# Performance work log

Hardware: AMD Instinct MI355X
Metric: run time of the kernel (lower is better)

Reference implementation:

```python
import jax, jax.numpy as jnp
import numpy as np
from jax import lax

B, C, H, W = 16, 256, 32, 32
HK, WK = 16, 16
NH = 8              # num_heads
HD = C // NH        # head_dim = 32
N = H * W           # 1024
M = HK * WK         # 256
EXP = 3             # attn_expansion
HID = NH * EXP      # 24 hidden channels in DLA
EPS = 1e-5


def setup_inputs() -> dict:
    key = jax.random.key(0)
    ks = jax.random.split(key, 16)
    s = 0.02
    return {
        "q": jax.random.normal(ks[0], (B, C, H, W), jnp.float32),
        "kv": jax.random.normal(ks[1], (B, C, HK, WK), jnp.float32),
        "Wq": jax.random.normal(ks[2], (C, C), jnp.float32) * s,
        "Wkv": jax.random.normal(ks[3], (2 * C, C), jnp.float32) * s,
        "Wp": jax.random.normal(ks[4], (C, C), jnp.float32) * s,
        "bp": jnp.zeros((C,), jnp.float32),
        "rpb": jnp.ones((N, M), jnp.float32),
        "W_exp": jax.random.normal(ks[5], (HID, NH), jnp.float32) * s,   # 1x1 conv heads->hidden
        "g1": jnp.ones((HID,), jnp.float32),
        "b1": jnp.zeros((HID,), jnp.float32),
        "W_dw": jax.random.normal(ks[6], (HID, 1, 3, 3), jnp.float32) * s,  # depthwise 3x3
        "g2": jnp.ones((HID,), jnp.float32),
        "b2": jnp.zeros((HID,), jnp.float32),
        "W_red": jax.random.normal(ks[7], (NH, HID), jnp.float32) * s,  # 1x1 conv hidden->heads
        "g3": jnp.ones((NH,), jnp.float32),
        "b3": jnp.zeros((NH,), jnp.float32),
    }


def group_norm(x, gamma, beta, groups):
    b, c, h, w = x.shape
    xg = x.reshape(b, groups, c // groups, h, w)
    mu = xg.mean(axis=(2, 3, 4), keepdims=True)
    var = xg.var(axis=(2, 3, 4), keepdims=True)
    xn = ((xg - mu) * lax.rsqrt(var + EPS)).reshape(b, c, h, w)
    return xn * gamma[None, :, None, None] + beta[None, :, None, None]


def swish(x):
    return x * jax.nn.sigmoid(x)


def dla(a, W_exp, g1, b1, W_dw, g2, b2, W_red, g3, b3):
    # a: [B, NH, N, M] treated as NCHW image with C=num_heads
    x = jnp.einsum('bcnm,oc->bonm', a, W_exp)              # 1x1 expand -> [B,HID,N,M]
    x = swish(group_norm(x, g1, b1, EXP))
    x = lax.conv_general_dilated(
        x, W_dw, window_strides=(1, 1), padding='SAME',
        feature_group_count=HID,
        dimension_numbers=('NCHW', 'OIHW', 'NCHW'))        # depthwise 3x3
    x = swish(group_norm(x, g2, b2, EXP))
    x = jnp.einsum('bcnm,oc->bonm', x, W_red)              # 1x1 reduce -> [B,NH,N,M]
    x = group_norm(x, g3, b3, 1)                            # no activation
    return x


def reference(q, kv, Wq, Wkv, Wp, bp, rpb, W_exp, g1, b1, W_dw, g2, b2, W_red, g3, b3):
    b = q.shape[0]
    scale = HD ** -0.5
    # kv path: [B,C,HK,WK] -> [B,M,C] -> Linear(C->2C)
    kv_t = kv.reshape(b, C, M).transpose(0, 2, 1)
    kvp = kv_t @ Wkv.T                                     # [B,M,2C]
    kvp = kvp.reshape(b, M, 2, NH, HD).transpose(2, 0, 3, 1, 4)  # [2,B,NH,M,HD]
    k, v = kvp[0], kvp[1]
    # q path: [B,C,H,W] -> [B,N,C] -> Linear -> [B,NH,N,HD]
    qf = (q.reshape(b, C, N).transpose(0, 2, 1) @ Wq.T)
    qh = qf.reshape(b, N, NH, HD).transpose(0, 2, 1, 3)
    attn = jnp.einsum('bhnd,bhmd->bhnm', qh, k) * scale + rpb[None, None]
    attn = jax.nn.softmax(attn, axis=-1)
    attn = dla(attn, W_exp, g1, b1, W_dw, g2, b2, W_red, g3, b3)
    out = jnp.einsum('bhnm,bhmd->bhnd', attn, v)           # [B,NH,N,HD]
    out = out.transpose(0, 2, 1, 3).reshape(b, N, C)
    out = out @ Wp.T + bp
    return out.transpose(0, 2, 1).reshape(b, C, H, W)
```

## Files before the change

### kernel.cpp

```cpp
#include <hip/hip_runtime.h>
#include <math.h>

#define Bb 16
#define Cc 256
#define Nn 1024
#define Mm 256
#define NHh 8
#define HDd 32
#define HIDh 24
#define NMs (Nn*Mm)
#define TTB 16
#define CHUNK 8
#define EPSf 1e-5f
#define SCALEf 0.17677669529663687f
#define STP 32

typedef float v2f __attribute__((ext_vector_type(2)));
typedef __attribute__((ext_vector_type(8))) short bf8v;
typedef __attribute__((ext_vector_type(4))) float f4v;

__device__ __forceinline__ float wave_sum(float v){
#pragma unroll
  for (int off=32; off; off>>=1) v += __shfl_xor(v, off, 64);
  return v;
}
__device__ __forceinline__ float wave_max(float v){
#pragma unroll
  for (int off=32; off; off>>=1) v = fmaxf(v, __shfl_xor(v, off, 64));
  return v;
}
__device__ __forceinline__ float sigm_(float x){ return __builtin_amdgcn_rcpf(1.f + __expf(-x)); }
__device__ __forceinline__ float swish_(float x){ return x * sigm_(x); }
__device__ __forceinline__ v2f swish2(v2f x){
  v2f r;
  r.x = x.x * sigm_(x.x);
  r.y = x.y * sigm_(x.y);
  return r;
}
__device__ __forceinline__ unsigned short f2bf(float f){
  unsigned u = __float_as_uint(f);
  u += 0x7fffu + ((u >> 16) & 1u);
  return (unsigned short)(u >> 16);
}
__device__ __forceinline__ unsigned cvtpk(float lo, float hi){
  unsigned r;
  asm("v_cvt_pk_bf16_f32 %0, %1, %2" : "=v"(r) : "v"(lo), "v"(hi));
  return r;
}
__device__ __forceinline__ float bfup(unsigned short s){ return __uint_as_float(((unsigned)s) << 16); }
__device__ __forceinline__ float bflo(unsigned u){ return __uint_as_float(u << 16); }
__device__ __forceinline__ float bfhi(unsigned u){ return __uint_as_float(u & 0xffff0000u); }
__device__ __forceinline__ void gload_lds16(const void* g, void* l){
  __builtin_amdgcn_global_load_lds(
      (const __attribute__((address_space(1))) unsigned int*)g,
      (__attribute__((address_space(3))) unsigned int*)l, 16, 0, 0);
}

template<int HASBIAS>
__launch_bounds__(256)
__global__ void gemm_mfma(const float* __restrict__ A,
                          const float* __restrict__ W,
                          const float* __restrict__ bias,
                          float* __restrict__ O)
{
  __shared__ __align__(16) unsigned short Wt[64 * 40];
  __shared__ __align__(16) unsigned short At[64 * 40];
  const int b = blockIdx.z;
  const int i0 = blockIdx.x * 64;
  const int j0 = blockIdx.y * 64;
  const int tid = threadIdx.x;
  const int lane = tid & 63, wv = tid >> 6;
  const int wj = (wv >> 1) * 32, wi = (wv & 1) * 32;
  const int l15 = lane & 15, l4 = lane >> 4;

  const float* Ab = A + (long)b * Cc * Nn;
  const int sj = tid >> 2, skh = (tid & 3) * 8;
  const int si = tid & 63, skb = (tid >> 6) * 8;

  f4v acc[2][2] = {};
  for (int k0 = 0; k0 < Cc; k0 += 32) {
    float wreg[8];
    {
      const float* wp = W + (long)(j0 + sj) * Cc + k0 + skh;
      *(f4v*)&wreg[0] = *(const f4v*)&wp[0];
      *(f4v*)&wreg[4] = *(const f4v*)&wp[4];
    }
    float areg[8];
    {
      const float* ap = Ab + (long)(k0 + skb) * Nn + i0 + si;
#pragma unroll
      for (int e = 0; e < 8; e++) areg[e] = ap[(long)e * Nn];
    }
    __syncthreads();
    {
      unsigned pk[4];
#pragma unroll
      for (int t = 0; t < 4; t++) pk[t] = cvtpk(wreg[2*t], wreg[2*t+1]);
      *(uint4*)&Wt[sj*40 + skh] = make_uint4(pk[0], pk[1], pk[2], pk[3]);
#pragma unroll
      for (int t = 0; t < 4; t++) pk[t] = cvtpk(areg[2*t], areg[2*t+1]);
      *(uint4*)&At[si*40 + skb] = make_uint4(pk[0], pk[1], pk[2], pk[3]);
    }
    __syncthreads();
    bf8v af[2], bf[2];
#pragma unroll
    for (int fm = 0; fm < 2; fm++)
      af[fm] = *(const bf8v*)&Wt[(wj + fm*16 + l15)*40 + l4*8];
#pragma unroll
    for (int fn = 0; fn < 2; fn++)
      bf[fn] = *(const bf8v*)&At[(wi + fn*16 + l15)*40 + l4*8];
#pragma unroll
    for (int fm = 0; fm < 2; fm++)
#pragma unroll
      for (int fn = 0; fn < 2; fn++)
        acc[fm][fn] = __builtin_amdgcn_mfma_f32_16x16x32_bf16(af[fm], bf[fn], acc[fm][fn], 0, 0, 0);
  }
#pragma unroll
  for (int fm = 0; fm < 2; fm++) {
    f4v bv = {0.f, 0.f, 0.f, 0.f};
    if (HASBIAS) bv = *(const f4v*)&bias[j0 + wj + fm*16 + l4*4];
#pragma unroll
    for (int fn = 0; fn < 2; fn++) {
      const int jj = j0 + wj + fm*16 + l4*4;
      const int ii = i0 + wi + fn*16 + l15;
      float* op = O + ((long)b * Cc + jj) * Nn + ii;
#pragma unroll
      for (int r = 0; r < 4; r++)
        op[(long)r * Nn] = acc[fm][fn][r] + bv[r];
    }
  }
}

template<int MODE>
__launch_bounds__(256)
__global__ void gemm_tn(const float* __restrict__ A, const float* __restrict__ W,
                        const float* __restrict__ bias, float* __restrict__ O1,
                        float* __restrict__ O2, int Kdim, long sAb, int sAk, int sAi)
{
  __shared__ __align__(16) float As[16][68];
  __shared__ __align__(16) float Ws[16][68];
  const int b  = blockIdx.z;
  const int i0 = blockIdx.x * 64;
  const int j0 = blockIdx.y * 64;
  const int tid = threadIdx.x;
  const int tx = tid & 15, ty = tid >> 4;
  const float* Ab = A + (long)b * sAb;
  float acc[4][4] = {};
  for (int k0 = 0; k0 < Kdim; k0 += 16) {
#pragma unroll
    for (int t = 0; t < 4; t++) {
      int idx = tid + t * 256;
      int kk, ii;
      if (sAi == 1) { kk = idx >> 6; ii = idx & 63; }
      else          { ii = idx >> 4; kk = idx & 15; }
      As[kk][ii] = Ab[(long)(k0 + kk) * sAk + (long)(i0 + ii) * sAi];
    }
#pragma unroll
    for (int t = 0; t < 4; t++) {
      int idx = tid + t * 256;
      int jj = idx & 63, kk = idx >> 6;
      Ws[kk][jj] = W[(long)(j0 + jj) * Kdim + (k0 + kk)];
    }
    __syncthreads();
#pragma unroll
    for (int kk = 0; kk < 16; kk++) {
      const float4 av = *(const float4*)&As[kk][tx * 4];
      const float4 wv = *(const float4*)&Ws[kk][ty * 4];
      const float a4[4] = {av.x, av.y, av.z, av.w};
      const float w4[4] = {wv.x, wv.y, wv.z, wv.w};
#pragma unroll
      for (int u = 0; u < 4; u++)
#pragma unroll
        for (int v = 0; v < 4; v++)
          acc[u][v] = fmaf(a4[u], w4[v], acc[u][v]);
    }
    __syncthreads();
  }
#pragma unroll
  for (int v = 0; v < 4; v++) {
    const int j = j0 + ty * 4 + v;
    const int two = j >> 8, jj = j & 255;
    const int h = jj >> 5, d = jj & 31;
    float* p = two ? O2 : O1;
#pragma unroll
    for (int u = 0; u < 4; u++)
      p[(((long)b * NHh + h) * Mm + (i0 + tx * 4 + u)) * HDd + d] = acc[u][v];
  }
}

__launch_bounds__(256)
__global__ void compute_sv(const float* __restrict__ vb, float* __restrict__ sv)
{
  __shared__ float red[256];
  const int bh = blockIdx.x, tid = threadIdx.x;
  const int d = tid & 31, ch = tid >> 5;
  const float* vp = vb + (long)bh * Mm * HDd;
  float s = 0.f;
  for (int m = ch; m < Mm; m += 8) s += vp[m * HDd + d];
  red[tid] = s;
  __syncthreads();
  if (tid < 32) {
    float t = 0.f;
#pragma unroll
    for (int cc = 0; cc < 8; cc++) t += red[cc * 32 + tid];
    sv[(long)bh * HDd + tid] = t;
  }
}

__launch_bounds__(256)
__global__ void attn_softmax(const float* __restrict__ qhT, const float* __restrict__ kb,
                             const float* __restrict__ rpb, unsigned short* __restrict__ attn)
{
  __shared__ __align__(16) float Ks[Mm][36];
  __shared__ __align__(16) float qs[32][36];
  const int b = blockIdx.z, h = blockIdx.y, n0 = blockIdx.x * 32;
  const int tid = threadIdx.x;
  const float* kp = kb + ((long)b * NHh + h) * Mm * HDd;
#pragma unroll
  for (int u = 0; u < 8; u++) {
    const int f = tid + u * 256;
    const int m = f >> 3, d = (f & 7) * 4;
    *(float4*)&Ks[m][d] = *(const float4*)&kp[m * HDd + d];
  }
  const float* qp = qhT + ((long)b * NHh + h) * HDd * Nn;
#pragma unroll
  for (int u = 0; u < 4; u++) {
    const int idx = tid + u * 256;
    const int nn = idx & 31, dd = idx >> 5;
    qs[nn][dd] = qp[(long)dd * Nn + n0 + nn];
  }
  __syncthreads();
  const int lane = tid & 63, w = tid >> 6;
  const int r0 = w * 8;
  float s[8][4] = {};
#pragma unroll
  for (int dq = 0; dq < 8; dq++) {
    float4 k4[4];
#pragma unroll
    for (int j = 0; j < 4; j++) k4[j] = *(const float4*)&Ks[lane + j * 64][dq * 4];
#pragma unroll
    for (int r = 0; r < 8; r++) {
      const float4 q4 = *(const float4*)&qs[r0 + r][dq * 4];
#pragma unroll
      for (int j = 0; j < 4; j++) {
        s[r][j] = fmaf(q4.x, k4[j].x, s[r][j]);
        s[r][j] = fmaf(q4.y, k4[j].y, s[r][j]);
        s[r][j] = fmaf(q4.z, k4[j].z, s[r][j]);
        s[r][j] = fmaf(q4.w, k4[j].w, s[r][j]);
      }
    }
  }
#pragma unroll
  for (int r = 0; r < 8; r++) {
    const int n = n0 + r0 + r;
    const float* rp = rpb + (long)n * Mm;
    float sc[4];
#pragma unroll
    for (int j = 0; j < 4; j++) sc[j] = fmaf(s[r][j], SCALEf, rp[lane + j * 64]);
    float mx = fmaxf(fmaxf(sc[0], sc[1]), fmaxf(sc[2], sc[3]));
    mx = wave_max(mx);
    float e[4], sum = 0.f;
#pragma unroll
    for (int j = 0; j < 4; j++) { e[j] = __expf(sc[j] - mx); sum += e[j]; }
    sum = wave_sum(sum);
    const float inv = __builtin_amdgcn_rcpf(sum);
    unsigned short* ap = attn + (((long)b * NHh + h) * Nn + n) * Mm;
#pragma unroll
    for (int j = 0; j < 4; j++) ap[lane + j * 64] = f2bf(e[j] * inv);
  }
}

__launch_bounds__(256)
__global__ void gram_stats(const unsigned short* __restrict__ attn, float* __restrict__ G)
{
  __shared__ float red[36][4];
  const int b = blockIdx.y, tid = threadIdx.x;
  const unsigned short* ap = attn + (long)b * NHh * NMs + (long)blockIdx.x * 2048 + tid * 8;
  float a[8][8];
#pragma unroll
  for (int h = 0; h < 8; h++) {
    const uint4 v = *(const uint4*)&ap[(long)h * NMs];
    a[h][0] = bflo(v.x); a[h][1] = bfhi(v.x); a[h][2] = bflo(v.y); a[h][3] = bfhi(v.y);
    a[h][4] = bflo(v.z); a[h][5] = bfhi(v.z); a[h][6] = bflo(v.w); a[h][7] = bfhi(v.w);
  }
  float g[36];
  int t = 0;
#pragma unroll
  for (int i = 0; i < 8; i++)
#pragma unroll
    for (int j = i; j < 8; j++, t++) {
      float s = 0.f;
#pragma unroll
      for (int m = 0; m < 8; m++) s = fmaf(a[i][m], a[j][m], s);
      g[t] = s;
    }
  const int lane = tid & 63, wid = tid >> 6;
#pragma unroll
  for (int t2 = 0; t2 < 36; t2++) {
    const float s = wave_sum(g[t2]);
    if (lane == 0) red[t2][wid] = s;
  }
  __syncthreads();
  if (tid < 36)
    atomicAdd(&G[((long)b * 36 + tid) * STP],
              red[tid][0] + red[tid][1] + red[tid][2] + red[tid][3]);
}

__launch_bounds__(768, 6)
__global__ void dla_pass_b(const unsigned short* __restrict__ attn,
                           const float* __restrict__ Wexp,
                           const float* __restrict__ g1, const float* __restrict__ b1,
                           const float* __restrict__ G, const float* __restrict__ Wdw,
                           unsigned short* __restrict__ x2, float* __restrict__ stats2c, int b0)
{
  __shared__ __align__(16) unsigned short sl[(TTB + 2) * NHh * Mm];
  const int tid = threadIdx.x;
  const int wv = tid >> 6, lane = tid & 63;
  const int bc = blockIdx.y, b = b0 + bc;
  const int n0 = blockIdx.x * TTB;
  const int c0 = wv * 2;
  const int g = wv >> 2;

  {
    const unsigned short* abase = attn + (long)b * NHh * NMs;
    const int q_lo = lane >> 5;
    const int m0 = (lane & 31) * 8;
#pragma unroll
    for (int i = 0; i < 6; i++) {
      const int pp = (wv * 6 + i) * 2;
      const int row = pp >> 3;
      const int nn = n0 - 1 + row;
      if (nn >= 0 && nn < Nn) {
        const int h = (pp + q_lo) & 7;
        gload_lds16(abase + (long)h * NMs + (long)nn * Mm + m0, &sl[pp * Mm]);
      }
    }
  }

  float mu, rs;
  {
    const float* Gb = G + (long)b * 36 * STP;
    float sum = 0.f, sumsq = 0.f;
    for (int c = g * 8; c < g * 8 + 8; c++) {
      float w[8];
#pragma unroll
      for (int h = 0; h < 8; h++) w[h] = Wexp[c * 8 + h];
      float wsu = 0.f;
#pragma unroll
      for (int h = 0; h < 8; h++) wsu += w[h];
      sum += wsu;
      float s2 = 0.f;
      int t = 0;
#pragma unroll
      for (int i = 0; i < 8; i++)
#pragma unroll
        for (int j = i; j < 8; j++, t++) {
          const float f = (i == j) ? 1.f : 2.f;
          s2 = fmaf(f * w[i] * w[j], Gb[t * STP], s2);
        }
      sumsq += s2;
    }
    const float cnt = 8.f * NMs;
    mu = sum * ((float)Nn / cnt);
    const float var = sumsq / cnt - mu * mu;
    rs = rsqrtf(var + EPSf);
  }
  v2f we2[8], wd2[9], B12;
  {
    const float A10 = rs * g1[c0], A11 = rs * g1[c0 + 1];
    B12.x = b1[c0] - mu * A10;
    B12.y = b1[c0 + 1] - mu * A11;
#pragma unroll
    for (int h = 0; h < NHh; h++) {
      we2[h].x = Wexp[c0 * NHh + h] * A10;
      we2[h].y = Wexp[(c0 + 1) * NHh + h] * A11;
    }
#pragma unroll
    for (int k = 0; k < 9; k++) {
      wd2[k].x = Wdw[c0 * 9 + k];
      wd2[k].y = Wdw[(c0 + 1) * 9 + k];
    }
  }
  __syncthreads();

  v2f s1p[4] = {}, s2p[4] = {};
  v2f smp = {0.f, 0.f}, sqp = {0.f, 0.f};
  for (int r = -1; r <= TTB; r++) {
    const int nn = n0 + r;
    const bool rowv = (nn >= 0 && nn < Nn);
    v2f xp[4];
    if (rowv) {
#pragma unroll
      for (int mi = 0; mi < 4; mi++) xp[mi] = B12;
      const unsigned short* sp = &sl[(r + 1) * NHh * Mm + lane * 4];
#pragma unroll
      for (int h = 0; h < NHh; h++) {
        const ushort4 v = *(const ushort4*)&sp[h * Mm];
        xp[0] += we2[h] * bfup(v.x);
        xp[1] += we2[h] * bfup(v.y);
        xp[2] += we2[h] * bfup(v.z);
        xp[3] += we2[h] * bfup(v.w);
      }
#pragma unroll
      for (int mi = 0; mi < 4; mi++) xp[mi] = swish2(xp[mi]);
    } else {
#pragma unroll
      for (int mi = 0; mi < 4; mi++) xp[mi] = (v2f){0.f, 0.f};
    }
    v2f xl, xr;
    xl.x = __shfl_up(xp[3].x, 1);  xl.y = __shfl_up(xp[3].y, 1);
    xr.x = __shfl_down(xp[0].x, 1); xr.y = __shfl_down(xp[0].y, 1);
    if (lane == 0)  { xl = (v2f){0.f, 0.f}; }
    if (lane == 63) { xr = (v2f){0.f, 0.f}; }
    const v2f L[4] = {xl, xp[0], xp[1], xp[2]};
    const v2f R[4] = {xp[1], xp[2], xp[3], xr};
    v2f y[4];
#pragma unroll
    for (int mi = 0; mi < 4; mi++) {
      const v2f u0 = wd2[0] * L[mi] + wd2[1] * xp[mi] + wd2[2] * R[mi];
      const v2f u1 = wd2[3] * L[mi] + wd2[4] * xp[mi] + wd2[5] * R[mi];
      const v2f u2 = wd2[6] * L[mi] + wd2[7] * xp[mi] + wd2[8] * R[mi];
      y[mi] = s2p[mi] + u2;
      s2p[mi] = s1p[mi] + u1;
      s1p[mi] = u0;
    }
    if (r >= 1) {
#pragma unroll
      for (int mi = 0; mi < 4; mi++) {
        smp += y[mi];
        sqp += y[mi] * y[mi];
      }
      const int nw = n0 + r - 1;
      const unsigned w0 = cvtpk(y[0].x, y[1].x), w1 = cvtpk(y[2].x, y[3].x);
      const unsigned w2 = cvtpk(y[0].y, y[1].y), w3 = cvtpk(y[2].y, y[3].y);
      unsigned short* xq = x2 + ((long)(bc * Nn + nw) * HIDh + c0) * Mm + lane * 4;
      *(uint2*)xq        = make_uint2(w0, w1);
      *(uint2*)(xq + Mm) = make_uint2(w2, w3);
    }
  }
  {
    const float vs0 = wave_sum(smp.x), vq0 = wave_sum(sqp.x);
    const float vs1 = wave_sum(smp.y), vq1 = wave_sum(sqp.y);
    if (lane == 0) {
      atomicAdd(&stats2c[((long)b * HIDh + c0) * STP], vs0);
      atomicAdd(&stats2c[((long)b * HIDh + c0) * STP + 1], vq0);
      atomicAdd(&stats2c[((long)b * HIDh + c0 + 1) * STP], vs1);
      atomicAdd(&stats2c[((long)b * HIDh + c0 + 1) * STP + 1], vq1);
    }
  }
}

__launch_bounds__(256)
__global__ void dla_pass_c(const unsigned short* __restrict__ x2, const float* __restrict__ g2,
                           const float* __restrict__ b2, const float* __restrict__ stats2c,
                           const float* __restrict__ Wred, unsigned short* __restrict__ a2,
                           float* __restrict__ partial3, int b0)
{
  __shared__ float wA[HIDh], wB[HIDh], wrs[HIDh][NHh];
  __shared__ float red2[2][4];
  const int tid = threadIdx.x;
  const int wv = tid >> 6, lane = tid & 63;
  const int bc = blockIdx.y, b = b0 + bc;
  if (tid < HIDh) {
    const int c = tid, g = c >> 3;
    float s = 0.f, q = 0.f;
#pragma unroll
    for (int cc = 0; cc < 8; cc++) {
      s += stats2c[((long)b * HIDh + g * 8 + cc) * STP];
      q += stats2c[((long)b * HIDh + g * 8 + cc) * STP + 1];
    }
    const float cnt = 8.f * NMs;
    const float mu = s / cnt;
    const float var = q / cnt - mu * mu;
    const float A2 = rsqrtf(var + EPSf) * g2[c];
    wA[c] = A2; wB[c] = b2[c] - mu * A2;
  }
  if (tid < HIDh * NHh) {
    const int c = tid >> 3, h = tid & 7;
    wrs[c][h] = Wred[h * HIDh + c];
  }
  __syncthreads();
  const int rsel = lane >> 5, ms = lane & 31;
  const int n = blockIdx.x * 8 + wv * 2 + rsel;
  const unsigned short* xp = x2 + (long)(bc * Nn + n) * HIDh * Mm + ms * 8;
  float red[NHh][8] = {};
#pragma unroll
  for (int c = 0; c < HIDh; c++) {
    const uint4 xv = *(const uint4*)&xp[c * Mm];
    const float Ac = wA[c], Bc = wB[c];
    float sw[8];
    sw[0] = swish_(fmaf(bflo(xv.x), Ac, Bc));
    sw[1] = swish_(fmaf(bfhi(xv.x), Ac, Bc));
    sw[2] = swish_(fmaf(bflo(xv.y), Ac, Bc));
    sw[3] = swish_(fmaf(bfhi(xv.y), Ac, Bc));
    sw[4] = swish_(fmaf(bflo(xv.z), Ac, Bc));
    sw[5] = swish_(fmaf(bfhi(xv.z), Ac, Bc));
    sw[6] = swish_(fmaf(bflo(xv.w), Ac, Bc));
    sw[7] = swish_(fmaf(bfhi(xv.w), Ac, Bc));
#pragma unroll
    for (int h = 0; h < NHh; h++) {
      const float w = wrs[c][h];
#pragma unroll
      for (int mi = 0; mi < 8; mi++) red[h][mi] = fmaf(w, sw[mi], red[h][mi]);
    }
  }
  float s3 = 0.f, q3 = 0.f;
#pragma unroll
  for (int h = 0; h < NHh; h++) {
    uint4 st;
    st.x = cvtpk(red[h][0], red[h][1]);
    st.y = cvtpk(red[h][2], red[h][3]);
    st.z = cvtpk(red[h][4], red[h][5]);
    st.w = cvtpk(red[h][6], red[h][7]);
    *(uint4*)&a2[(((long)b * NHh + h) * Nn + n) * Mm + ms * 8] = st;
#pragma unroll
    for (int mi = 0; mi < 8; mi++) {
      s3 += red[h][mi]; q3 = fmaf(red[h][mi], red[h][mi], q3);
    }
  }
  s3 = wave_sum(s3); q3 = wave_sum(q3);
  if (lane == 0) { red2[0][wv] = s3; red2[1][wv] = q3; }
  __syncthreads();
  if (tid < 2) {
    float t = red2[tid][0] + red2[tid][1] + red2[tid][2] + red2[tid][3];
    partial3[((long)b * 128 + blockIdx.x) * 2 + tid] = t;
  }
}

__launch_bounds__(128)
__global__ void finalize_stats3(const float* __restrict__ partial3, float* __restrict__ stats3)
{
  __shared__ float red2[2][2];
  const int b = blockIdx.x, tid = threadIdx.x;
  const int lane = tid & 63, wv = tid >> 6;
  float s = partial3[((long)b * 128 + tid) * 2];
  float q = partial3[((long)b * 128 + tid) * 2 + 1];
  s = wave_sum(s); q = wave_sum(q);
  if (lane == 0) { red2[0][wv] = s; red2[1][wv] = q; }
  __syncthreads();
  if (tid < 2)
    stats3[b * 2 + tid] = red2[tid][0] + red2[tid][1];
}

__launch_bounds__(256)
__global__ void pv_mfma(const unsigned short* __restrict__ a2, const float* __restrict__ vb,
                        const float* __restrict__ sv, const float* __restrict__ stats3,
                        const float* __restrict__ g3, const float* __restrict__ b3,
                        float* __restrict__ o)
{
  __shared__ __align__(16) unsigned short Vt[32 * 264];
  const int b = blockIdx.z, h = blockIdx.y, n0 = blockIdx.x * 128;
  const int tid = threadIdx.x;
  const int lane = tid & 63, wv = tid >> 6;
  const int l15 = lane & 15, l4 = lane >> 4;
  {
    const float* vp = vb + ((long)b * NHh + h) * Mm * HDd;
#pragma unroll
    for (int u = 0; u < 32; u++) {
      const int idx = tid + u * 256;
      const int m = idx >> 5, d = idx & 31;
      Vt[d * 264 + m] = f2bf(vp[idx]);
    }
  }
  __syncthreads();
  const unsigned short* ap = a2 + (((long)b * NHh + h) * Nn + n0) * Mm;
  f4v acc[2][2] = {};
#pragma unroll 2
  for (int k0 = 0; k0 < Mm; k0 += 32) {
    bf8v af[2], bf[2];
#pragma unroll
    for (int fm = 0; fm < 2; fm++)
      af[fm] = *(const bf8v*)&Vt[(fm * 16 + l15) * 264 + k0 + l4 * 8];
#pragma unroll
    for (int fn = 0; fn < 2; fn++)
      bf[fn] = *(const bf8v*)&ap[(long)(wv * 32 + fn * 16 + l15) * Mm + k0 + l4 * 8];
#pragma unroll
    for (int fm = 0; fm < 2; fm++)
#pragma unroll
      for (int fn = 0; fn < 2; fn++)
        acc[fm][fn] = __builtin_amdgcn_mfma_f32_16x16x32_bf16(af[fm], bf[fn], acc[fm][fn], 0, 0, 0);
  }
  const float cnt = (float)(NHh * NMs);
  const float mu = stats3[b * 2] / cnt;
  const float var = stats3[b * 2 + 1] / cnt - mu * mu;
  const float r3 = rsqrtf(var + EPSf);
  const float alpha = r3 * g3[h];
  const float beta = b3[h] - mu * alpha;
#pragma unroll
  for (int fm = 0; fm < 2; fm++) {
#pragma unroll
    for (int r = 0; r < 4; r++) {
      const int d = fm * 16 + l4 * 4 + r;
      const float bv = beta * sv[((long)b * NHh + h) * HDd + d];
      float* op = o + ((long)b * Cc + h * HDd + d) * Nn + n0 + wv * 32 + l15;
#pragma unroll
      for (int fn = 0; fn < 2; fn++)
        op[fn * 16] = fmaf(alpha, acc[fm][fn][r], bv);
    }
  }
}

extern "C" void kernel_launch(void* const* d_in, const int* in_sizes, int n_in,
                              void* d_out, int out_size, void* d_ws, size_t ws_size,
                              hipStream_t stream) {
  const float* q    = (const float*)d_in[0];
  const float* kv   = (const float*)d_in[1];
  const float* Wq   = (const float*)d_in[2];
  const float* Wkv  = (const float*)d_in[3];
  const float* Wp   = (const float*)d_in[4];
  const float* bp   = (const float*)d_in[5];
  const float* rpb  = (const float*)d_in[6];
  const float* Wexp = (const float*)d_in[7];
  const float* g1   = (const float*)d_in[8];
  const float* b1   = (const float*)d_in[9];
  const float* Wdw  = (const float*)d_in[10];
  const float* g2   = (const float*)d_in[11];
  const float* b2   = (const float*)d_in[12];
  const float* Wred = (const float*)d_in[13];
  const float* g3   = (const float*)d_in[14];
  const float* b3   = (const float*)d_in[15];
  float* out = (float*)d_out;

  float* ws = (float*)d_ws;
  size_t off = 0;
  auto alloc = [&](size_t n) { float* p = ws + off; off += n; return p; };
  float* attnf   = alloc((size_t)Bb * NHh * NMs / 2);
  float* a2f     = alloc((size_t)Bb * NHh * NMs / 2);
  float* big     = alloc((size_t)CHUNK * HIDh * NMs / 2);
  float* kbuf    = alloc((size_t)Bb * NHh * Mm * HDd);
  float* vbuf    = alloc((size_t)Bb * NHh * Mm * HDd);
  float* sv      = alloc((size_t)Bb * NHh * HDd);
  float* G       = alloc((size_t)Bb * 36 * STP);
  float* stats2c = alloc((size_t)Bb * HIDh * STP);
  float* stats3  = alloc(Bb * 2);
  float* partial3= alloc((size_t)Bb * 128 * 2);
  unsigned short* attn = (unsigned short*)attnf;
  unsigned short* a2 = (unsigned short*)a2f;
  float* qhT = big;
  unsigned short* x2 = (unsigned short*)big;
  float* oT = big;

  hipMemsetAsync(G, 0, (size_t)(Bb * 36 * STP + Bb * HIDh * STP) * sizeof(float), stream);

  gemm_mfma<0><<<dim3(Nn / 64, Cc / 64, Bb), 256, 0, stream>>>(q, Wq, nullptr, qhT);
  gemm_tn<1><<<dim3(Mm / 64, 512 / 64, Bb), 256, 0, stream>>>(
      kv, Wkv, nullptr, kbuf, vbuf, Cc, (long)Cc * Mm, Mm, 1);
  compute_sv<<<dim3(Bb * NHh), 256, 0, stream>>>(vbuf, sv);
  attn_softmax<<<dim3(Nn / 32, NHh, Bb), 256, 0, stream>>>(qhT, kbuf, rpb, attn);
  gram_stats<<<dim3(NMs / 2048, Bb), 256, 0, stream>>>(attn, G);

  for (int b0 = 0; b0 < Bb; b0 += CHUNK) {
    dla_pass_b<<<dim3(Nn / TTB, CHUNK), 768, 0, stream>>>(
        attn, Wexp, g1, b1, G, Wdw, x2, stats2c, b0);
    dla_pass_c<<<dim3(Nn / 8, CHUNK), 256, 0, stream>>>(
        x2, g2, b2, stats2c, Wred, a2, partial3, b0);
  }
  finalize_stats3<<<dim3(Bb), 128, 0, stream>>>(partial3, stats3);

  pv_mfma<<<dim3(Nn / 128, NHh, Bb), 256, 0, stream>>>(a2, vbuf, sv, stats3, g3, b3, oT);
  gemm_mfma<1><<<dim3(Nn / 64, Cc / 64, Bb), 256, 0, stream>>>(oT, Wp, bp, out);
}
```

Measured before the change: 423.1 us.

## Use bf16 MFMA for QK^T softmax kernel and shrink DLA tile rows

The attention-score kernel now converts K and Q to bf16 in LDS and computes QK^T with 16x16x32 bf16 MFMA instead of scalar FP32 FMAs. Each block handles 64 query rows, and the softmax reductions use cross-lane shuffles adapted to the MFMA output layout. Writes are packed bf16 vector stores. Separately, the DLA pass tile height TTB drops from 16 to 8, with the halo load loop rewritten to match. The changes trade score precision (bf16 inputs) for matrix-core throughput, and give the DLA pass more, smaller blocks at the cost of relatively more halo traffic.

```diff
diff --git a/kernel.cpp b/kernel.cpp
--- a/kernel.cpp
+++ b/kernel.cpp
@@ -9,7 +9,7 @@
 #define HDd 32
 #define HIDh 24
 #define NMs (Nn*Mm)
-#define TTB 16
+#define TTB 8
 #define CHUNK 8
 #define EPSf 1e-5f
 #define SCALEf 0.17677669529663687f
@@ -22,11 +22,6 @@
 __device__ __forceinline__ float wave_sum(float v){
 #pragma unroll
   for (int off=32; off; off>>=1) v += __shfl_xor(v, off, 64);
-  return v;
-}
-__device__ __forceinline__ float wave_max(float v){
-#pragma unroll
-  for (int off=32; off; off>>=1) v = fmaxf(v, __shfl_xor(v, off, 64));
   return v;
 }
 __device__ __forceinline__ float sigm_(float x){ return __builtin_amdgcn_rcpf(1.f + __expf(-x)); }
@@ -211,62 +206,74 @@
 __global__ void attn_softmax(const float* __restrict__ qhT, const float* __restrict__ kb,
                              const float* __restrict__ rpb, unsigned short* __restrict__ attn)
 {
-  __shared__ __align__(16) float Ks[Mm][36];
-  __shared__ __align__(16) float qs[32][36];
-  const int b = blockIdx.z, h = blockIdx.y, n0 = blockIdx.x * 32;
+  __shared__ __align__(16) unsigned short Kt[Mm * 40];
+  __shared__ __align__(16) unsigned short Qt[64 * 40];
+  const int b = blockIdx.z, h = blockIdx.y, n0 = blockIdx.x * 64;
   const int tid = threadIdx.x;
-  const float* kp = kb + ((long)b * NHh + h) * Mm * HDd;
-#pragma unroll
-  for (int u = 0; u < 8; u++) {
-    const int f = tid + u * 256;
-    const int m = f >> 3, d = (f & 7) * 4;
-    *(float4*)&Ks[m][d] = *(const float4*)&kp[m * HDd + d];
-  }
-  const float* qp = qhT + ((long)b * NHh + h) * HDd * Nn;
-#pragma unroll
-  for (int u = 0; u < 4; u++) {
-    const int idx = tid + u * 256;
-    const int nn = idx & 31, dd = idx >> 5;
-    qs[nn][dd] = qp[(long)dd * Nn + n0 + nn];
-  }
-  __syncthreads();
-  const int lane = tid & 63, w = tid >> 6;
-  const int r0 = w * 8;
-  float s[8][4] = {};
-#pragma unroll
-  for (int dq = 0; dq < 8; dq++) {
-    float4 k4[4];
-#pragma unroll
-    for (int j = 0; j < 4; j++) k4[j] = *(const float4*)&Ks[lane + j * 64][dq * 4];
-#pragma unroll
-    for (int r = 0; r < 8; r++) {
-      const float4 q4 = *(const float4*)&qs[r0 + r][dq * 4];
-#pragma unroll
-      for (int j = 0; j < 4; j++) {
-        s[r][j] = fmaf(q4.x, k4[j].x, s[r][j]);
-        s[r][j] = fmaf(q4.y, k4[j].y, s[r][j]);
-        s[r][j] = fmaf(q4.z, k4[j].z, s[r][j]);
-        s[r][j] = fmaf(q4.w, k4[j].w, s[r][j]);
-      }
-    }
-  }
-#pragma unroll
-  for (int r = 0; r < 8; r++) {
-    const int n = n0 + r0 + r;
-    const float* rp = rpb + (long)n * Mm;
-    float sc[4];
-#pragma unroll
-    for (int j = 0; j < 4; j++) sc[j] = fmaf(s[r][j], SCALEf, rp[lane + j * 64]);
-    float mx = fmaxf(fmaxf(sc[0], sc[1]), fmaxf(sc[2], sc[3]));
-    mx = wave_max(mx);
-    float e[4], sum = 0.f;
-#pragma unroll
-    for (int j = 0; j < 4; j++) { e[j] = __expf(sc[j] - mx); sum += e[j]; }
-    sum = wave_sum(sum);
-    const float inv = __builtin_amdgcn_rcpf(sum);
-    unsigned short* ap = attn + (((long)b * NHh + h) * Nn + n) * Mm;
-#pragma unroll
-    for (int j = 0; j < 4; j++) ap[lane + j * 64] = f2bf(e[j] * inv);
+  const int lane = tid & 63, wv = tid >> 6;
+  const int l15 = lane & 15, l4 = lane >> 4;
+  {
+    const float* kp = kb + ((long)b * NHh + h) * Mm * HDd;
+#pragma unroll
+    for (int u = 0; u < 8; u++) {
+      const int f = tid + u * 256;
+      const int m = f >> 3, dq = (f & 7) * 4;
+      const f4v k4 = *(const f4v*)&kp[m * HDd + dq];
+      *(uint2*)&Kt[m * 40 + dq] = make_uint2(cvtpk(k4.x, k4.y), cvtpk(k4.z, k4.w));
+    }
+  }
+  {
+    const float* qp = qhT + ((long)b * NHh + h) * HDd * Nn + n0;
+#pragma unroll
+    for (int u = 0; u < 4; u++) {
+      const int f = tid + u * 256;
+      const int n = f & 63, d2 = (f >> 6) * 2;
+      const float q0 = qp[(long)d2 * Nn + n];
+      const float q1 = qp[(long)(d2 + 1) * Nn + n];
+      *(unsigned*)&Qt[n * 40 + d2] = cvtpk(q0, q1);
+    }
+  }
+  __syncthreads();
+  const bf8v qf = *(const bf8v*)&Qt[(wv * 16 + l15) * 40 + l4 * 8];
+  f4v S[16];
+#pragma unroll
+  for (int mt = 0; mt < 16; mt++) {
+    const bf8v kf = *(const bf8v*)&Kt[(mt * 16 + l15) * 40 + l4 * 8];
+    f4v z = {0.f, 0.f, 0.f, 0.f};
+    S[mt] = __builtin_amdgcn_mfma_f32_16x16x32_bf16(kf, qf, z, 0, 0, 0);
+  }
+  const int n = n0 + wv * 16 + l15;
+  const float* rp = rpb + (long)n * Mm;
+  float mx = -1e30f;
+#pragma unroll
+  for (int mt = 0; mt < 16; mt++) {
+    const f4v r4 = *(const f4v*)&rp[mt * 16 + l4 * 4];
+    S[mt][0] = fmaf(S[mt][0], SCALEf, r4.x);
+    S[mt][1] = fmaf(S[mt][1], SCALEf, r4.y);
+    S[mt][2] = fmaf(S[mt][2], SCALEf, r4.z);
+    S[mt][3] = fmaf(S[mt][3], SCALEf, r4.w);
+    mx = fmaxf(mx, fmaxf(fmaxf(S[mt][0], S[mt][1]), fmaxf(S[mt][2], S[mt][3])));
+  }
+  mx = fmaxf(mx, __shfl_xor(mx, 16, 64));
+  mx = fmaxf(mx, __shfl_xor(mx, 32, 64));
+  float sum = 0.f;
+#pragma unroll
+  for (int mt = 0; mt < 16; mt++) {
+    S[mt][0] = __expf(S[mt][0] - mx);
+    S[mt][1] = __expf(S[mt][1] - mx);
+    S[mt][2] = __expf(S[mt][2] - mx);
+    S[mt][3] = __expf(S[mt][3] - mx);
+    sum += (S[mt][0] + S[mt][1]) + (S[mt][2] + S[mt][3]);
+  }
+  sum += __shfl_xor(sum, 16, 64);
+  sum += __shfl_xor(sum, 32, 64);
+  const float inv = __builtin_amdgcn_rcpf(sum);
+  unsigned short* ap = attn + (((long)b * NHh + h) * Nn + n) * Mm;
+#pragma unroll
+  for (int mt = 0; mt < 16; mt++) {
+    const unsigned p0 = cvtpk(S[mt][0] * inv, S[mt][1] * inv);
+    const unsigned p1 = cvtpk(S[mt][2] * inv, S[mt][3] * inv);
+    *(uint2*)&ap[mt * 16 + l4 * 4] = make_uint2(p0, p1);
   }
 }
 
@@ -326,13 +333,16 @@
     const int q_lo = lane >> 5;
     const int m0 = (lane & 31) * 8;
 #pragma unroll
-    for (int i = 0; i < 6; i++) {
-      const int pp = (wv * 6 + i) * 2;
-      const int row = pp >> 3;
-      const int nn = n0 - 1 + row;
-      if (nn >= 0 && nn < Nn) {
-        const int h = (pp + q_lo) & 7;
-        gload_lds16(abase + (long)h * NMs + (long)nn * Mm + m0, &sl[pp * Mm]);
+    for (int i = 0; i < 4; i++) {
+      const int pr = wv + i * 12;
+      if (pr < 40) {
+        const int pp = pr * 2;
+        const int row = pp >> 3;
+        const int nn = n0 - 1 + row;
+        if (nn >= 0 && nn < Nn) {
+          const int h = (pp + q_lo) & 7;
+          gload_lds16(abase + (long)h * NMs + (long)nn * Mm + m0, &sl[pp * Mm]);
+        }
       }
     }
   }
@@ -646,7 +656,7 @@
   gemm_tn<1><<<dim3(Mm / 64, 512 / 64, Bb), 256, 0, stream>>>(
       kv, Wkv, nullptr, kbuf, vbuf, Cc, (long)Cc * Mm, Mm, 1);
   compute_sv<<<dim3(Bb * NHh), 256, 0, stream>>>(vbuf, sv);
-  attn_softmax<<<dim3(Nn / 32, NHh, Bb), 256, 0, stream>>>(qhT, kbuf, rpb, attn);
+  attn_softmax<<<dim3(Nn / 64, NHh, Bb), 256, 0, stream>>>(qhT, kbuf, rpb, attn);
   gram_stats<<<dim3(NMs / 2048, Bb), 256, 0, stream>>>(attn, G);
 
   for (int b0 = 0; b0 < Bb; b0 += CHUNK) {
```

Result: slower. 433.5 us (+2.5%).
